# Kernel optimization log

Measured on AMD Instinct MI355X. Metric: run time of the kernel, lower is better.

Reference implementation:

```python
import jax, jax.numpy as jnp
import numpy as np
from jax import lax
from jax.scipy.special import gammaln

N, H, W = 16, 1080, 1920
NUM_SV = 600
KS, KSIG = 7, 7.0 / 6.0
GAMMA_NP = np.arange(0.2, 10.0 + 0.001, 0.001, dtype=np.float64).astype(np.float32)

FEATURE_RANGES = jnp.asarray([[0.338, 10], [0.017204, 0.806612], [0.236, 1.642], [-0.123884, 0.20293], [0.000155, 0.712298], [0.001122, 0.470257], [0.244, 1.641], [-0.123586, 0.179083], [0.000152, 0.710456], [0.000975, 0.470984], [0.249, 1.555], [-0.135687, 0.100858], [0.000174, 0.684173], [0.000913, 0.534174], [0.258, 1.561], [-0.143408, 0.100486], [0.000179, 0.685696], [0.000888, 0.536508], [0.471, 3.264], [0.012809, 0.703171], [0.218, 1.046], [-0.094876, 0.187459], [1.5e-05, 0.442057], [0.001272, 0.40803], [0.222, 1.042], [-0.115772, 0.162604], [1.6e-05, 0.444362], [0.001374, 0.40243], [0.227, 0.996], [-0.117188, 0.098323], [3e-05, 0.531903], [0.001122, 0.369589], [0.228, 0.99], [-0.12243, 0.098658], [2.8e-05, 0.530092], [0.001118, 0.370399]], dtype=jnp.float32)


def _gauss_kernel():
    ax = np.arange(KS, dtype=np.float64) - (KS - 1) / 2
    g = np.exp(-(ax ** 2) / (2 * KSIG ** 2))
    k = np.outer(g, g)
    k /= k.sum()
    return jnp.asarray(k, jnp.float32)


def _cubic(x):
    ax = np.abs(x); ax2 = ax * ax; ax3 = ax2 * ax
    return (1.5 * ax3 - 2.5 * ax2 + 1) * (ax <= 1) + (-0.5 * ax3 + 2.5 * ax2 - 4 * ax + 2) * ((ax > 1) & (ax <= 2))


def _resize_matrix(in_len, scale=0.5):
    # Matlab-style antialiased bicubic downscale weights as a dense (out,in) matrix.
    out_len = int(np.ceil(in_len * scale))
    kw = 4.0 / scale
    u = (np.arange(1, out_len + 1, dtype=np.float64) / scale) + 0.5 * (1 - 1 / scale)
    left = np.floor(u - kw / 2)
    P = int(np.ceil(kw)) + 2
    ind = left[:, None] + np.arange(P)[None, :]  # 1-based
    w = scale * _cubic((u[:, None] - ind) * scale)
    w = w / w.sum(1, keepdims=True)
    aux = np.concatenate([np.arange(in_len), np.arange(in_len)[::-1]])  # symmetric boundary
    idx = aux[np.mod(ind.astype(np.int64) - 1, 2 * in_len)]
    M = np.zeros((out_len, in_len), np.float64)
    np.add.at(M, (np.repeat(np.arange(out_len), P), idx.ravel()), w.ravel())
    return jnp.asarray(M, jnp.float32)


def imresize_half(x):
    Mh = _resize_matrix(x.shape[-2])
    Mw = _resize_matrix(x.shape[-1])
    x = jnp.einsum('oh,nchw->ncow', Mh, x)
    return jnp.einsum('pw,ncow->ncop', Mw, x)


def normalize_img_with_gauss(x):
    k = _gauss_kernel()[None, None]  # (1,1,7,7)
    conv = lambda z: lax.conv_general_dilated(z, k, (1, 1), 'SAME', dimension_numbers=('NCHW', 'OIHW', 'NCHW'))
    mu = conv(x)
    sigma = jnp.sqrt(jnp.abs(conv(x * x) - mu * mu) + 1e-8)
    return (x - mu) / (sigma + 1.0)


def _tables():
    g = jnp.asarray(GAMMA_NP)
    r = jnp.exp(2 * gammaln(2.0 / g) - gammaln(1.0 / g) - gammaln(3.0 / g))
    return g, r


def estimate_ggd(x):
    g, r = _tables()
    s2 = jnp.mean(x * x, axis=(1, 2, 3))
    E = jnp.mean(jnp.abs(x), axis=(1, 2, 3))
    rho = s2 / (E * E)
    idx = jnp.argmin(jnp.abs(rho[:, None] - r[None, :]), axis=-1)
    return g[idx], jnp.sqrt(s2)


def estimate_aggd(x):
    g, r = _tables()
    ml = (x < 0).astype(x.dtype)
    mr = (x > 0).astype(x.dtype)
    cl = jnp.sum(ml, (1, 2, 3))
    cr = jnp.sum(mr, (1, 2, 3))
    sl = jnp.sqrt(jnp.sum((x * ml) ** 2, (1, 2, 3)) / cl)
    sr = jnp.sqrt(jnp.sum((x * mr) ** 2, (1, 2, 3)) / cr)
    gh = sl / sr
    rhat = jnp.mean(jnp.abs(x), (1, 2, 3)) ** 2 / jnp.mean(x * x, (1, 2, 3))
    rhn = rhat * (gh ** 3 + 1) * (gh + 1) / (gh ** 2 + 1) ** 2
    idx = jnp.argmin(jnp.abs(r[None, :] - rhn[:, None]), axis=-1)
    return g[idx], sl, sr


def natural_scene_statistics(luma):
    xn = normalize_img_with_gauss(luma)
    a, s = estimate_ggd(xn)
    feats = [a, s * s]
    for sh in ((0, 1), (1, 0), (1, 1), (-1, 1)):
        xs = jnp.roll(xn, sh, axis=(-2, -1))
        a, sl, sr = estimate_aggd(xn * xs)
        eta = (sr - sl) * jnp.exp(gammaln(2.0 / a) - (gammaln(1.0 / a) + gammaln(3.0 / a)) / 2)
        feats += [a, eta, sl * sl, sr * sr]
    return jnp.stack(feats, -1)  # (N,18)


def setup_inputs() -> dict:
    key = jax.random.key(0)
    k1, k2, k3 = jax.random.split(key, 3)
    x = jax.random.uniform(k1, (N, 3, H, W), jnp.float32)
    sv = jax.random.normal(k2, (NUM_SV, 36), jnp.float32)
    sv_coef = jax.random.normal(k3, (NUM_SV,), jnp.float32)
    return {'x': x, 'sv': sv, 'sv_coef': sv_coef}


def reference(x, sv, sv_coef):
    # Y channel (YIQ luma, pyiqa default), scaled to [0,255]
    y = jnp.einsum('nchw,c->nhw', x, jnp.asarray([0.299, 0.587, 0.114], x.dtype))[:, None] * 255.0
    f1 = natural_scene_statistics(y)
    f2 = natural_scene_statistics(imresize_half(y))
    f = jnp.concatenate([f1, f2], axis=-1)  # (N,36)
    lo = FEATURE_RANGES[:, 0]
    hi = FEATURE_RANGES[:, 1]
    sf = -1.0 + 2.0 * (f - lo) / (hi - lo)
    dist = jnp.sum((sf[:, :, None] - sv.T[None, :, :]) ** 2, axis=1)  # (N,num_sv)
    kf = jnp.exp(-0.05 * dist)
    return kf @ sv_coef + 153.591  # score = kf@coef - rho, rho=-153.591
```

## Files before the change

### kernel.cpp

```cpp
#include <hip/hip_runtime.h>
#include <math.h>

#define NIMG 16
#define FH 1080
#define FW 1920
#define HHh 540
#define HWw 960
#define FHW (FH*FW)
#define TMPW (HHh*FW)
#define HHW (HHh*HWw)
#define NG 9801

struct GW { float w[7]; };

__device__ const float FR[36][2] = {
 {0.338f, 10.f}, {0.017204f, 0.806612f}, {0.236f, 1.642f}, {-0.123884f, 0.20293f},
 {0.000155f, 0.712298f}, {0.001122f, 0.470257f}, {0.244f, 1.641f}, {-0.123586f, 0.179083f},
 {0.000152f, 0.710456f}, {0.000975f, 0.470984f}, {0.249f, 1.555f}, {-0.135687f, 0.100858f},
 {0.000174f, 0.684173f}, {0.000913f, 0.534174f}, {0.258f, 1.561f}, {-0.143408f, 0.100486f},
 {0.000179f, 0.685696f}, {0.000888f, 0.536508f}, {0.471f, 3.264f}, {0.012809f, 0.703171f},
 {0.218f, 1.046f}, {-0.094876f, 0.187459f}, {1.5e-05f, 0.442057f}, {0.001272f, 0.40803f},
 {0.222f, 1.042f}, {-0.115772f, 0.162604f}, {1.6e-05f, 0.444362f}, {0.001374f, 0.40243f},
 {0.227f, 0.996f}, {-0.117188f, 0.098323f}, {3e-05f, 0.531903f}, {0.001122f, 0.369589f},
 {0.228f, 0.99f}, {-0.12243f, 0.098658f}, {2.8e-05f, 0.530092f}, {0.001118f, 0.370399f}
};

__global__ void k_zero(float* p, int n){
  int i = blockIdx.x*blockDim.x + threadIdx.x;
  if (i < n) p[i] = 0.f;
}

__global__ __launch_bounds__(256) void k_luma(const float* __restrict__ x, float* __restrict__ y, int n0, int nb){
  long long idx = (long long)blockIdx.x*blockDim.x + threadIdx.x;
  long long tot = (long long)nb*(FHW/4);
  if (idx >= tot) return;
  int n = (int)(idx / (FHW/4));
  int p = (int)(idx - (long long)n*(FHW/4));
  const float4* base = (const float4*)(x + (long long)(n0+n)*3*FHW);
  float4 r = base[p];
  float4 g = base[p + FHW/4];
  float4 b = base[p + 2*(FHW/4)];
  float4 o;
  o.x = 255.0f*(0.299f*r.x + 0.587f*g.x + 0.114f*b.x);
  o.y = 255.0f*(0.299f*r.y + 0.587f*g.y + 0.114f*b.y);
  o.z = 255.0f*(0.299f*r.z + 0.587f*g.z + 0.114f*b.z);
  o.w = 255.0f*(0.299f*r.w + 0.587f*g.w + 0.114f*b.w);
  ((float4*)(y + (long long)n*FHW))[p] = o;
}

__global__ __launch_bounds__(256) void k_gnorm(const float* __restrict__ src, float* __restrict__ dst,
                                               int Hi, int Wi, GW gw){
  __shared__ float ly[38][40];
  __shared__ float hs[38][33];
  __shared__ float h2[38][33];
  int n = blockIdx.z;
  const float* im = src + (long long)n*Hi*Wi;
  float* om = dst + (long long)n*Hi*Wi;
  int bx = blockIdx.x*32, by = blockIdx.y*32;
  int tid = threadIdx.x;
  for (int t = tid; t < 38*38; t += 256){
    int r = t / 38, c = t - r*38;
    int gi = by + r - 3, gj = bx + c - 3;
    float v = 0.f;
    if (gi >= 0 && gi < Hi && gj >= 0 && gj < Wi) v = im[(long long)gi*Wi + gj];
    ly[r][c] = v;
  }
  __syncthreads();
  for (int t = tid; t < 38*32; t += 256){
    int r = t >> 5, c = t & 31;
    float s = 0.f, s2 = 0.f;
    #pragma unroll
    for (int k = 0; k < 7; k++){ float v = ly[r][c+k]; s += gw.w[k]*v; s2 += gw.w[k]*v*v; }
    hs[r][c] = s; h2[r][c] = s2;
  }
  __syncthreads();
  int c = tid & 31, r0 = tid >> 5;
  for (int r = r0; r < 32; r += 8){
    float mu = 0.f, m2 = 0.f;
    #pragma unroll
    for (int k = 0; k < 7; k++){ mu += gw.w[k]*hs[r+k][c]; m2 += gw.w[k]*h2[r+k][c]; }
    int gi = by + r, gj = bx + c;
    if (gi < Hi && gj < Wi){
      float yv = ly[r+3][c+3];
      float sig = sqrtf(fabsf(m2 - mu*mu) + 1e-8f);
      om[(long long)gi*Wi + gj] = (yv - mu)/(sig + 1.0f);
    }
  }
}

__global__ __launch_bounds__(256) void k_nss(const float* __restrict__ xn, float* __restrict__ acc,
                                             int Hi, int Wi, int accBase){
  int n = blockIdx.y;
  const float* img = xn + (long long)n*Hi*Wi;
  float a[22];
  #pragma unroll
  for (int k = 0; k < 22; k++) a[k] = 0.f;
  for (int i = blockIdx.x; i < Hi; i += gridDim.x){
    const float* rc = img + (long long)i*Wi;
    const float* rm = img + (long long)((i==0)?(Hi-1):(i-1))*Wi;
    const float* rp = img + (long long)((i==Hi-1)?0:(i+1))*Wi;
    for (int j = threadIdx.x; j < Wi; j += 256){
      int jm = (j==0)?(Wi-1):(j-1);
      float xc = rc[j];
      float xl = rc[jm], xu = rm[j], xul = rm[jm], xdl = rp[jm];
      a[0] += xc*xc;
      a[1] += fabsf(xc);
      float pr[4] = {xc*xl, xc*xu, xc*xul, xc*xdl};
      #pragma unroll
      for (int k = 0; k < 4; k++){
        float pp = pr[k];
        float q = pp*pp;
        if (pp < 0.f){ a[2+5*k] += 1.f; a[4+5*k] += q; }
        else if (pp > 0.f){ a[3+5*k] += 1.f; a[5+5*k] += q; }
        a[6+5*k] += fabsf(pp);
      }
    }
  }
  __shared__ float wsum[4][22];
  int lane = threadIdx.x & 63, wv = threadIdx.x >> 6;
  #pragma unroll
  for (int k = 0; k < 22; k++){
    float v = a[k];
    for (int off = 32; off > 0; off >>= 1) v += __shfl_down(v, off, 64);
    if (lane == 0) wsum[wv][k] = v;
  }
  __syncthreads();
  if (threadIdx.x < 22){
    float s = wsum[0][threadIdx.x]+wsum[1][threadIdx.x]+wsum[2][threadIdx.x]+wsum[3][threadIdx.x];
    atomicAdd(&acc[accBase + n*22 + threadIdx.x], s);
  }
}

__device__ double d_cubic(double x){
  double ax = fabs(x), ax2 = ax*ax, ax3 = ax2*ax;
  if (ax <= 1.0) return 1.5*ax3 - 2.5*ax2 + 1.0;
  if (ax <= 2.0) return -0.5*ax3 + 2.5*ax2 - 4.0*ax + 2.0;
  return 0.0;
}

__global__ void k_rsetup(float* __restrict__ wH, int* __restrict__ iH,
                         float* __restrict__ wW, int* __restrict__ iW){
  int t = blockIdx.x*blockDim.x + threadIdx.x;
  int inl, o; float* wp; int* ip;
  if (t < HHh){ inl = FH; wp = wH; ip = iH; o = t; }
  else if (t < HHh + HWw){ inl = FW; wp = wW; ip = iW; o = t - HHh; }
  else return;
  double u = 2.0*(o+1) - 0.5;
  double left = floor(u - 4.0);
  double wv[10]; int idx[10]; double s = 0.0;
  for (int p = 0; p < 10; p++){
    double ind = left + p;
    double xv = (u - ind)*0.5;
    double w = 0.5*d_cubic(xv);
    wv[p] = w; s += w;
    long long L2 = 2*(long long)inl;
    long long m = (long long)ind - 1;
    m = ((m % L2) + L2) % L2;
    idx[p] = (m < inl) ? (int)m : (int)(L2 - 1 - m);
  }
  for (int p = 0; p < 10; p++){
    wp[o*10+p] = (float)(wv[p]/s);
    ip[o*10+p] = idx[p];
  }
}

__global__ __launch_bounds__(256) void k_resizeh(const float* __restrict__ y, float* __restrict__ tmp,
                                                 const float* __restrict__ wH, const int* __restrict__ iH, int nb){
  int t = blockIdx.x*blockDim.x + threadIdx.x;
  int tot = nb*HHh*(FW/4);
  if (t >= tot) return;
  int j = t % (FW/4);
  int o = (t / (FW/4)) % HHh;
  int n = t / (HHh*(FW/4));
  const float* yi = y + (long long)n*FHW;
  float4 s = {0.f,0.f,0.f,0.f};
  for (int p = 0; p < 10; p++){
    float w = wH[o*10+p];
    int r = iH[o*10+p];
    float4 v = ((const float4*)(yi + (long long)r*FW))[j];
    s.x += w*v.x; s.y += w*v.y; s.z += w*v.z; s.w += w*v.w;
  }
  ((float4*)(tmp + (long long)n*TMPW))[o*(FW/4)+j] = s;
}

__global__ __launch_bounds__(256) void k_resizew(const float* __restrict__ tmp, float* __restrict__ yh,
                                                 const float* __restrict__ wW, const int* __restrict__ iW, int nb){
  int t = blockIdx.x*blockDim.x + threadIdx.x;
  int tot = nb*HHW;
  if (t >= tot) return;
  int q = t % HWw;
  int o = (t / HWw) % HHh;
  int n = t / HHW;
  const float* row = tmp + (long long)n*TMPW + (long long)o*FW;
  float s = 0.f;
  for (int p = 0; p < 10; p++) s += wW[q*10+p]*row[iW[q*10+p]];
  yh[(long long)n*HHW + (long long)o*HWw + q] = s;
}

__global__ void k_rtab(float* __restrict__ rt){
  int i = blockIdx.x*blockDim.x + threadIdx.x;
  if (i >= NG) return;
  float g = (float)(0.2 + 0.001*(double)i);
  double gd = (double)g;
  double r = exp(2.0*lgamma(2.0/gd) - lgamma(1.0/gd) - lgamma(3.0/gd));
  rt[i] = (float)r;
}

__global__ __launch_bounds__(256) void k_final(const float* __restrict__ acc, const float* __restrict__ rt,
                                               const float* __restrict__ sv, const float* __restrict__ coef,
                                               float* __restrict__ out){
  int n = blockIdx.x;
  __shared__ float targ[10];
  __shared__ float sfs[36];
  __shared__ int argi[10];
  __shared__ float slv[8], srv[8], feat[36];
  __shared__ float rbv[4]; __shared__ int rbi[4];
  __shared__ float ws2[4];
  int tid = threadIdx.x;
  if (tid == 0){
    for (int s = 0; s < 2; s++){
      const float* A = acc + (s*NIMG + n)*22;
      double HWs = s ? (double)HHW : (double)FHW;
      double s2m = A[0]/HWs;
      double Em  = A[1]/HWs;
      targ[s*5+0] = (float)(s2m/(Em*Em));
      feat[s*18+1] = (float)s2m;
      for (int k = 0; k < 4; k++){
        double cl = A[2+5*k], cr = A[3+5*k], sl2 = A[4+5*k], sr2 = A[5+5*k], sab = A[6+5*k];
        double sl = sqrt(sl2/cl), sr = sqrt(sr2/cr);
        double gh = sl/sr;
        double rhat = (sab/HWs)*(sab/HWs)/((sl2+sr2)/HWs);
        double rhn = rhat*(gh*gh*gh + 1.0)*(gh + 1.0)/((gh*gh + 1.0)*(gh*gh + 1.0));
        targ[s*5+1+k] = (float)rhn;
        slv[s*4+k] = (float)sl; srv[s*4+k] = (float)sr;
        feat[s*18+2+4*k+2] = (float)(sl2/cl);
        feat[s*18+2+4*k+3] = (float)(sr2/cr);
      }
    }
  }
  __syncthreads();
  for (int tix = 0; tix < 10; tix++){
    float tv = targ[tix];
    float bv = 3.4e38f; int bi = 0;
    for (int i = tid; i < NG; i += 256){
      float d = fabsf(tv - rt[i]);
      if (d < bv){ bv = d; bi = i; }
    }
    for (int off = 32; off > 0; off >>= 1){
      float ov = __shfl_down(bv, off, 64);
      int   oi = __shfl_down(bi, off, 64);
      if (ov < bv || (ov == bv && oi < bi)){ bv = ov; bi = oi; }
    }
    int lane = tid & 63, wv = tid >> 6;
    if (lane == 0){ rbv[wv] = bv; rbi[wv] = bi; }
    __syncthreads();
    if (tid == 0){
      for (int w = 1; w < 4; w++)
        if (rbv[w] < bv || (rbv[w] == bv && rbi[w] < bi)){ bv = rbv[w]; bi = rbi[w]; }
      argi[tix] = bi;
    }
    __syncthreads();
  }
  if (tid == 0){
    for (int s = 0; s < 2; s++){
      feat[s*18+0] = (float)(0.2 + 0.001*(double)argi[s*5]);
      for (int k = 0; k < 4; k++){
        double a = 0.2 + 0.001*(double)argi[s*5+1+k];
        double e = exp(lgamma(2.0/a) - 0.5*(lgamma(1.0/a) + lgamma(3.0/a)));
        feat[s*18+2+4*k+0] = (float)a;
        feat[s*18+2+4*k+1] = (float)(((double)srv[s*4+k] - (double)slv[s*4+k])*e);
      }
    }
    for (int i = 0; i < 36; i++){
      float lo = FR[i][0], hi = FR[i][1];
      sfs[i] = -1.0f + 2.0f*(feat[i]-lo)/(hi-lo);
    }
  }
  __syncthreads();
  float local = 0.f;
  for (int v = tid; v < 600; v += 256){
    float d = 0.f;
    #pragma unroll 4
    for (int i = 0; i < 36; i++){ float df = sfs[i] - sv[v*36+i]; d += df*df; }
    local += expf(-0.05f*d)*coef[v];
  }
  for (int off = 32; off > 0; off >>= 1) local += __shfl_down(local, off, 64);
  int lane = tid & 63, wv = tid >> 6;
  if (lane == 0) ws2[wv] = local;
  __syncthreads();
  if (tid == 0) out[n] = ws2[0]+ws2[1]+ws2[2]+ws2[3] + 153.591f;
}

extern "C" void kernel_launch(void* const* d_in, const int* in_sizes, int n_in,
                              void* d_out, int out_size, void* d_ws, size_t ws_size,
                              hipStream_t stream){
  const float* x    = (const float*)d_in[0];
  const float* sv   = (const float*)d_in[1];
  const float* coef = (const float*)d_in[2];
  float* out = (float*)d_out;
  char* ws = (char*)d_ws;

  float* acc = (float*)(ws + 0);
  float* rt  = (float*)(ws + 4096);
  float* wH  = (float*)(ws + 49152);
  int*   iH  = (int*)  (ws + 73728);
  float* wW  = (float*)(ws + 98304);
  int*   iW  = (int*)  (ws + 139264);
  float* Ybuf = (float*)(ws + 262144);

  size_t big = (ws_size > 262144) ? ws_size - 262144 : 0;
  int nbmax = (int)(big / (2ull*FHW*4));
  if (nbmax < 1) nbmax = 1;
  if (nbmax > NIMG) nbmax = NIMG;
  float* Bbuf = Ybuf + (size_t)nbmax*FHW;

  GW gw;
  {
    double g[7], s = 0.0;
    for (int k = 0; k < 7; k++){ double d = k - 3; g[k] = exp(-d*d/(2.0*(7.0/6.0)*(7.0/6.0))); s += g[k]; }
    for (int k = 0; k < 7; k++) gw.w[k] = (float)(g[k]/s);
  }

  k_zero<<<4, 256, 0, stream>>>(acc, 704);
  k_rtab<<<(NG+255)/256, 256, 0, stream>>>(rt);
  k_rsetup<<<(HHh+HWw+255)/256, 256, 0, stream>>>(wH, iH, wW, iW);

  for (int n0 = 0; n0 < NIMG; n0 += nbmax){
    int nb = (NIMG - n0 < nbmax) ? (NIMG - n0) : nbmax;
    {
      long long tot = (long long)nb*(FHW/4);
      k_luma<<<(int)((tot+255)/256), 256, 0, stream>>>(x, Ybuf, n0, nb);
    }
    {
      dim3 g2((FW+31)/32, (FH+31)/32, nb);
      k_gnorm<<<g2, 256, 0, stream>>>(Ybuf, Bbuf, FH, FW, gw);
    }
    k_nss<<<dim3(64, nb), 256, 0, stream>>>(Bbuf, acc, FH, FW, (0*NIMG + n0)*22);
    {
      int tot = nb*HHh*(FW/4);
      k_resizeh<<<(tot+255)/256, 256, 0, stream>>>(Ybuf, Bbuf, wH, iH, nb);
    }
    {
      int tot = nb*HHW;
      k_resizew<<<(tot+255)/256, 256, 0, stream>>>(Bbuf, Ybuf, wW, iW, nb);
    }
    float* XNH = Bbuf + (size_t)nbmax*TMPW;
    {
      dim3 g2((HWw+31)/32, (HHh+31)/32, nb);
      k_gnorm<<<g2, 256, 0, stream>>>(Ybuf, XNH, HHh, HWw, gw);
    }
    k_nss<<<dim3(64, nb), 256, 0, stream>>>(XNH, acc, HHh, HWw, (1*NIMG + n0)*22);
  }

  k_final<<<NIMG, 256, 0, stream>>>(acc, rt, sv, coef, out);
}
```

Measured before the change: 1.059 ms.

## Fuse Gaussian normalization with NSS statistics and fix wraparound borders separately

Merges the local-mean/variance normalization kernel and the paired-product statistics kernel into one tiled kernel. Each tile now computes a 34x34 normalized patch in shared memory and accumulates the 22 moments directly, so the normalized image is never written to or read back from global memory. Circular-wraparound border pairs are handled by a separate strip and fixup pass that recomputes the normalized values of the edge rows and columns. Atomics are spread over 32 slots per image to reduce contention, and the final kernel sums the slots. It also adds float4 tile loads for interior tiles. The cost is extra halo recompute per tile and more kernel launches for the small border passes.

```diff
diff --git a/kernel.cpp b/kernel.cpp
--- a/kernel.cpp
+++ b/kernel.cpp
@@ -10,6 +10,7 @@
 #define TMPW (HHh*FW)
 #define HHW (HHh*HWw)
 #define NG 9801
+#define NSLOT 32
 
 struct GW { float w[7]; };
 
@@ -48,86 +49,203 @@
   ((float4*)(y + (long long)n*FHW))[p] = o;
 }
 
-__global__ __launch_bounds__(256) void k_gnorm(const float* __restrict__ src, float* __restrict__ dst,
-                                               int Hi, int Wi, GW gw){
-  __shared__ float ly[38][40];
-  __shared__ float hs[38][33];
-  __shared__ float h2[38][33];
+__global__ __launch_bounds__(256) void k_fused(const float* __restrict__ src, float* __restrict__ acc,
+                                               int Hi, int Wi, int accBase, GW gw){
+  __shared__ float ly[40][48];
+  __shared__ float hs[40][36];
+  __shared__ float h2[40][36];
+  __shared__ float xs[34][36];
+  __shared__ float wsum[4][22];
   int n = blockIdx.z;
   const float* im = src + (long long)n*Hi*Wi;
-  float* om = dst + (long long)n*Hi*Wi;
   int bx = blockIdx.x*32, by = blockIdx.y*32;
   int tid = threadIdx.x;
-  for (int t = tid; t < 38*38; t += 256){
-    int r = t / 38, c = t - r*38;
-    int gi = by + r - 3, gj = bx + c - 3;
-    float v = 0.f;
-    if (gi >= 0 && gi < Hi && gj >= 0 && gj < Wi) v = im[(long long)gi*Wi + gj];
-    ly[r][c] = v;
-  }
-  __syncthreads();
-  for (int t = tid; t < 38*32; t += 256){
-    int r = t >> 5, c = t & 31;
-    float s = 0.f, s2 = 0.f;
-    #pragma unroll
-    for (int k = 0; k < 7; k++){ float v = ly[r][c+k]; s += gw.w[k]*v; s2 += gw.w[k]*v*v; }
-    hs[r][c] = s; h2[r][c] = s2;
-  }
-  __syncthreads();
-  int c = tid & 31, r0 = tid >> 5;
-  for (int r = r0; r < 32; r += 8){
-    float mu = 0.f, m2 = 0.f;
-    #pragma unroll
-    for (int k = 0; k < 7; k++){ mu += gw.w[k]*hs[r+k][c]; m2 += gw.w[k]*h2[r+k][c]; }
-    int gi = by + r, gj = bx + c;
-    if (gi < Hi && gj < Wi){
-      float yv = ly[r+3][c+3];
-      float sig = sqrtf(fabsf(m2 - mu*mu) + 1e-8f);
-      om[(long long)gi*Wi + gj] = (yv - mu)/(sig + 1.0f);
-    }
-  }
-}
-
-__global__ __launch_bounds__(256) void k_nss(const float* __restrict__ xn, float* __restrict__ acc,
-                                             int Hi, int Wi, int accBase){
+  bool fast = (bx >= 4) && (bx+36 <= Wi) && (by >= 4) && (by+36 <= Hi);
+  if (fast){
+    const float* base = im + (long long)(by-4)*Wi + (bx-4);
+    for (int t = tid; t < 400; t += 256){
+      int r = t/10, q = t-10*r;
+      float4 v = *(const float4*)(base + (long long)r*Wi + 4*q);
+      *(float4*)&ly[r][4*q] = v;
+    }
+  } else {
+    for (int t = tid; t < 1600; t += 256){
+      int r = t/40, c = t-40*r;
+      int gi = by-4+r, gj = bx-4+c;
+      float v = 0.f;
+      if (gi>=0 && gi<Hi && gj>=0 && gj<Wi) v = im[(long long)gi*Wi+gj];
+      ly[r][c] = v;
+    }
+  }
+  __syncthreads();
+  for (int t = tid; t < 360; t += 256){
+    int r = t/9, g = t-9*r; int c0 = 4*g;
+    float v[10];
+    #pragma unroll
+    for (int k=0;k<10;k++) v[k] = ly[r][c0+k];
+    #pragma unroll
+    for (int q=0;q<4;q++){
+      int cg = c0+q;
+      if (cg < 34){
+        float s=0.f, s2=0.f;
+        #pragma unroll
+        for (int k=0;k<7;k++){ float yv=v[q+k]; s += gw.w[k]*yv; s2 += gw.w[k]*yv*yv; }
+        hs[r][cg]=s; h2[r][cg]=s2;
+      }
+    }
+  }
+  __syncthreads();
+  for (int t = tid; t < 306; t += 256){
+    int rg0 = t/34, c = t-34*rg0; int r0 = 4*rg0;
+    float a[10], b[10];
+    #pragma unroll
+    for (int k=0;k<10;k++){
+      int rr = r0+k;
+      if (rr < 40){ a[k]=hs[rr][c]; b[k]=h2[rr][c]; } else { a[k]=0.f; b[k]=0.f; }
+    }
+    #pragma unroll
+    for (int q=0;q<4;q++){
+      int rg = r0+q;
+      if (rg < 34){
+        float mu=0.f, m2=0.f;
+        #pragma unroll
+        for (int k=0;k<7;k++){ mu += gw.w[k]*a[q+k]; m2 += gw.w[k]*b[q+k]; }
+        float yv = ly[rg+3][c+3];
+        float sig = sqrtf(fabsf(m2-mu*mu)+1e-8f);
+        xs[rg][c] = (yv-mu)/(sig+1.f);
+      }
+    }
+  }
+  __syncthreads();
+  float aR[22];
+  #pragma unroll
+  for (int k=0;k<22;k++) aR[k]=0.f;
+  {
+    int pc = tid & 31, rg = tid >> 5;
+    int r0 = 4*rg;
+    float xL[6], xC[6];
+    #pragma unroll
+    for (int k=0;k<6;k++){ xL[k]=xs[r0+k][pc]; xC[k]=xs[r0+k][pc+1]; }
+    int j = bx+pc;
+    #pragma unroll
+    for (int q=0;q<4;q++){
+      int i = by + r0 + q;
+      if (i < Hi && j < Wi){
+        float xc = xC[q+1];
+        aR[0] += xc*xc; aR[1] += fabsf(xc);
+        if (i != 0 && i != Hi-1 && j != 0){
+          float pr4[4] = { xc*xL[q+1], xc*xC[q], xc*xL[q], xc*xL[q+2] };
+          #pragma unroll
+          for (int k=0;k<4;k++){
+            float pp = pr4[k]; float qq = pp*pp;
+            if (pp<0.f){ aR[2+5*k]+=1.f; aR[4+5*k]+=qq; }
+            else if (pp>0.f){ aR[3+5*k]+=1.f; aR[5+5*k]+=qq; }
+            aR[6+5*k]+=fabsf(pp);
+          }
+        }
+      }
+    }
+  }
+  int lane = tid & 63, wv = tid >> 6;
+  #pragma unroll
+  for (int k=0;k<22;k++){
+    float v = aR[k];
+    for (int off=32; off>0; off>>=1) v += __shfl_down(v, off, 64);
+    if (lane==0) wsum[wv][k]=v;
+  }
+  __syncthreads();
+  if (tid < 22){
+    float s = wsum[0][tid]+wsum[1][tid]+wsum[2][tid]+wsum[3][tid];
+    int slot = (blockIdx.x + blockIdx.y) & (NSLOT-1);
+    atomicAdd(&acc[(((long long)(accBase + n))*NSLOT + slot)*22 + tid], s);
+  }
+}
+
+__device__ float xn_at(const float* __restrict__ im, int Hi, int Wi, int i, int j, const GW& gw){
+  float mu=0.f, m2=0.f;
+  for (int kr=-3;kr<=3;kr++){
+    int ii=i+kr; if (ii<0||ii>=Hi) continue;
+    float wr = gw.w[kr+3];
+    const float* row = im + (long long)ii*Wi;
+    for (int kc=-3;kc<=3;kc++){
+      int jj=j+kc; if (jj<0||jj>=Wi) continue;
+      float w = wr*gw.w[kc+3];
+      float yv = row[jj];
+      mu += w*yv; m2 += w*yv*yv;
+    }
+  }
+  float yv = im[(long long)i*Wi+j];
+  float sig = sqrtf(fabsf(m2-mu*mu)+1e-8f);
+  return (yv-mu)/(sig+1.f);
+}
+
+__global__ __launch_bounds__(256) void k_strips(const float* __restrict__ src, float* __restrict__ strip,
+                                                int Hi, int Wi, GW gw){
   int n = blockIdx.y;
-  const float* img = xn + (long long)n*Hi*Wi;
-  float a[22];
+  const float* im = src + (long long)n*Hi*Wi;
+  int C = 4*Wi + 2*Hi;
+  float* sb = strip + (long long)n*C;
+  for (int u = blockIdx.x*256 + threadIdx.x; u < C; u += gridDim.x*256){
+    int i, j;
+    if (u < 4*Wi){ int r=u/Wi; j=u-r*Wi; i = (r==0)?0:(r==1)?1:(r==2)?(Hi-2):(Hi-1); }
+    else { int v=u-4*Wi; int c=v/Hi; i=v-c*Hi; j = c?(Wi-1):0; }
+    sb[u] = xn_at(im, Hi, Wi, i, j, gw);
+  }
+}
+
+__device__ float strip_get(const float* __restrict__ sb, int Hi, int Wi, int i, int j){
+  if (i==0)    return sb[j];
+  if (i==1)    return sb[Wi+j];
+  if (i==Hi-2) return sb[2*Wi+j];
+  if (i==Hi-1) return sb[3*Wi+j];
+  if (j==0)    return sb[4*Wi+i];
+  return sb[4*Wi+Hi+i];
+}
+
+__global__ __launch_bounds__(256) void k_fixup(const float* __restrict__ strip, float* __restrict__ acc,
+                                               int Hi, int Wi, int accBase){
+  int n = blockIdx.y;
+  int C = 4*Wi + 2*Hi;
+  const float* sb = strip + (long long)n*C;
+  int nB = 2*Wi + Hi - 2;
+  float aR[20];
   #pragma unroll
-  for (int k = 0; k < 22; k++) a[k] = 0.f;
-  for (int i = blockIdx.x; i < Hi; i += gridDim.x){
-    const float* rc = img + (long long)i*Wi;
-    const float* rm = img + (long long)((i==0)?(Hi-1):(i-1))*Wi;
-    const float* rp = img + (long long)((i==Hi-1)?0:(i+1))*Wi;
-    for (int j = threadIdx.x; j < Wi; j += 256){
-      int jm = (j==0)?(Wi-1):(j-1);
-      float xc = rc[j];
-      float xl = rc[jm], xu = rm[j], xul = rm[jm], xdl = rp[jm];
-      a[0] += xc*xc;
-      a[1] += fabsf(xc);
-      float pr[4] = {xc*xl, xc*xu, xc*xul, xc*xdl};
-      #pragma unroll
-      for (int k = 0; k < 4; k++){
-        float pp = pr[k];
-        float q = pp*pp;
-        if (pp < 0.f){ a[2+5*k] += 1.f; a[4+5*k] += q; }
-        else if (pp > 0.f){ a[3+5*k] += 1.f; a[5+5*k] += q; }
-        a[6+5*k] += fabsf(pp);
-      }
-    }
-  }
-  __shared__ float wsum[4][22];
+  for (int k=0;k<20;k++) aR[k]=0.f;
+  for (int u = blockIdx.x*256 + threadIdx.x; u < nB; u += gridDim.x*256){
+    int i, j;
+    if (u < Wi){ i=0; j=u; }
+    else if (u < 2*Wi){ i=Hi-1; j=u-Wi; }
+    else { i = u-2*Wi+1; j=0; }
+    int jm = (j==0)?(Wi-1):(j-1);
+    int im_ = (i==0)?(Hi-1):(i-1);
+    int ip = (i==Hi-1)?0:(i+1);
+    float xc  = strip_get(sb,Hi,Wi,i,j);
+    float xl  = strip_get(sb,Hi,Wi,i,jm);
+    float xu  = strip_get(sb,Hi,Wi,im_,j);
+    float xul = strip_get(sb,Hi,Wi,im_,jm);
+    float xdl = strip_get(sb,Hi,Wi,ip,jm);
+    float pr4[4] = { xc*xl, xc*xu, xc*xul, xc*xdl };
+    #pragma unroll
+    for (int k=0;k<4;k++){
+      float pp = pr4[k]; float qq = pp*pp;
+      if (pp<0.f){ aR[0+5*k]+=1.f; aR[2+5*k]+=qq; }
+      else if (pp>0.f){ aR[1+5*k]+=1.f; aR[3+5*k]+=qq; }
+      aR[4+5*k]+=fabsf(pp);
+    }
+  }
+  __shared__ float wsum[4][20];
   int lane = threadIdx.x & 63, wv = threadIdx.x >> 6;
   #pragma unroll
-  for (int k = 0; k < 22; k++){
-    float v = a[k];
-    for (int off = 32; off > 0; off >>= 1) v += __shfl_down(v, off, 64);
-    if (lane == 0) wsum[wv][k] = v;
-  }
-  __syncthreads();
-  if (threadIdx.x < 22){
+  for (int k=0;k<20;k++){
+    float v = aR[k];
+    for (int off=32; off>0; off>>=1) v += __shfl_down(v, off, 64);
+    if (lane==0) wsum[wv][k]=v;
+  }
+  __syncthreads();
+  if (threadIdx.x < 20){
     float s = wsum[0][threadIdx.x]+wsum[1][threadIdx.x]+wsum[2][threadIdx.x]+wsum[3][threadIdx.x];
-    atomicAdd(&acc[accBase + n*22 + threadIdx.x], s);
+    int slot = blockIdx.x & (NSLOT-1);
+    atomicAdd(&acc[(((long long)(accBase + n))*NSLOT + slot)*22 + 2 + threadIdx.x], s);
   }
 }
 
@@ -210,6 +328,7 @@
                                                const float* __restrict__ sv, const float* __restrict__ coef,
                                                float* __restrict__ out){
   int n = blockIdx.x;
+  __shared__ float A[44];
   __shared__ float targ[10];
   __shared__ float sfs[36];
   __shared__ int argi[10];
@@ -217,16 +336,24 @@
   __shared__ float rbv[4]; __shared__ int rbi[4];
   __shared__ float ws2[4];
   int tid = threadIdx.x;
+  if (tid < 44){
+    int s = tid/22, k = tid-22*s;
+    const float* p = acc + (((long long)(s*NIMG + n))*NSLOT)*22 + k;
+    float sum = 0.f;
+    for (int sl = 0; sl < NSLOT; sl++) sum += p[sl*22];
+    A[tid] = sum;
+  }
+  __syncthreads();
   if (tid == 0){
     for (int s = 0; s < 2; s++){
-      const float* A = acc + (s*NIMG + n)*22;
+      const float* Ap = A + s*22;
       double HWs = s ? (double)HHW : (double)FHW;
-      double s2m = A[0]/HWs;
-      double Em  = A[1]/HWs;
+      double s2m = Ap[0]/HWs;
+      double Em  = Ap[1]/HWs;
       targ[s*5+0] = (float)(s2m/(Em*Em));
       feat[s*18+1] = (float)s2m;
       for (int k = 0; k < 4; k++){
-        double cl = A[2+5*k], cr = A[3+5*k], sl2 = A[4+5*k], sr2 = A[5+5*k], sab = A[6+5*k];
+        double cl = Ap[2+5*k], cr = Ap[3+5*k], sl2 = Ap[4+5*k], sr2 = Ap[5+5*k], sab = Ap[6+5*k];
         double sl = sqrt(sl2/cl), sr = sqrt(sr2/cr);
         double gh = sl/sr;
         double rhat = (sab/HWs)*(sab/HWs)/((sl2+sr2)/HWs);
@@ -300,19 +427,24 @@
   float* out = (float*)d_out;
   char* ws = (char*)d_ws;
 
-  float* acc = (float*)(ws + 0);
-  float* rt  = (float*)(ws + 4096);
-  float* wH  = (float*)(ws + 49152);
-  int*   iH  = (int*)  (ws + 73728);
-  float* wW  = (float*)(ws + 98304);
-  int*   iW  = (int*)  (ws + 139264);
-  float* Ybuf = (float*)(ws + 262144);
-
-  size_t big = (ws_size > 262144) ? ws_size - 262144 : 0;
-  int nbmax = (int)(big / (2ull*FHW*4));
+  float* acc    = (float*)(ws + 0);
+  float* rt     = (float*)(ws + 98304);
+  float* wH     = (float*)(ws + 139264);
+  int*   iH     = (int*)  (ws + 163840);
+  float* wW     = (float*)(ws + 188416);
+  int*   iW     = (int*)  (ws + 229376);
+  float* stripF = (float*)(ws + 270336);
+  float* stripH = (float*)(ws + 901120);
+  float* big    = (float*)(ws + 1310720);
+
+  size_t bigbytes = (ws_size > 1310720) ? ws_size - 1310720 : 0;
+  size_t perimg = (size_t)(FHW + TMPW + HHW)*4;
+  int nbmax = (int)(bigbytes / perimg);
   if (nbmax < 1) nbmax = 1;
   if (nbmax > NIMG) nbmax = NIMG;
-  float* Bbuf = Ybuf + (size_t)nbmax*FHW;
+  float* Ybuf = big;
+  float* Tbuf = Ybuf + (size_t)nbmax*FHW;
+  float* Hbuf = Tbuf + (size_t)nbmax*TMPW;
 
   GW gw;
   {
@@ -321,7 +453,7 @@
     for (int k = 0; k < 7; k++) gw.w[k] = (float)(g[k]/s);
   }
 
-  k_zero<<<4, 256, 0, stream>>>(acc, 704);
+  k_zero<<<(22528+255)/256, 256, 0, stream>>>(acc, 22528);
   k_rtab<<<(NG+255)/256, 256, 0, stream>>>(rt);
   k_rsetup<<<(HHh+HWw+255)/256, 256, 0, stream>>>(wH, iH, wW, iW);
 
@@ -333,23 +465,32 @@
     }
     {
       dim3 g2((FW+31)/32, (FH+31)/32, nb);
-      k_gnorm<<<g2, 256, 0, stream>>>(Ybuf, Bbuf, FH, FW, gw);
-    }
-    k_nss<<<dim3(64, nb), 256, 0, stream>>>(Bbuf, acc, FH, FW, (0*NIMG + n0)*22);
+      k_fused<<<g2, 256, 0, stream>>>(Ybuf, acc, FH, FW, 0*NIMG + n0, gw);
+    }
+    {
+      int C = 4*FW + 2*FH;
+      k_strips<<<dim3((C+255)/256, nb), 256, 0, stream>>>(Ybuf, stripF, FH, FW, gw);
+      int nB = 2*FW + FH - 2;
+      k_fixup<<<dim3((nB+255)/256, nb), 256, 0, stream>>>(stripF, acc, FH, FW, 0*NIMG + n0);
+    }
     {
       int tot = nb*HHh*(FW/4);
-      k_resizeh<<<(tot+255)/256, 256, 0, stream>>>(Ybuf, Bbuf, wH, iH, nb);
+      k_resizeh<<<(tot+255)/256, 256, 0, stream>>>(Ybuf, Tbuf, wH, iH, nb);
     }
     {
       int tot = nb*HHW;
-      k_resizew<<<(tot+255)/256, 256, 0, stream>>>(Bbuf, Ybuf, wW, iW, nb);
-    }
-    float* XNH = Bbuf + (size_t)nbmax*TMPW;
+      k_resizew<<<(tot+255)/256, 256, 0, stream>>>(Tbuf, Hbuf, wW, iW, nb);
+    }
     {
       dim3 g2((HWw+31)/32, (HHh+31)/32, nb);
-      k_gnorm<<<g2, 256, 0, stream>>>(Ybuf, XNH, HHh, HWw, gw);
-    }
-    k_nss<<<dim3(64, nb), 256, 0, stream>>>(XNH, acc, HHh, HWw, (1*NIMG + n0)*22);
+      k_fused<<<g2, 256, 0, stream>>>(Hbuf, acc, HHh, HWw, 1*NIMG + n0, gw);
+    }
+    {
+      int C = 4*HWw + 2*HHh;
+      k_strips<<<dim3((C+255)/256, nb), 256, 0, stream>>>(Hbuf, stripH, HHh, HWw, gw);
+      int nB = 2*HWw + HHh - 2;
+      k_fixup<<<dim3((nB+255)/256, nb), 256, 0, stream>>>(stripH, acc, HHh, HWw, 1*NIMG + n0);
+    }
   }
 
   k_final<<<NIMG, 256, 0, stream>>>(acc, rt, sv, coef, out);
```

New measurement: 1.192 ms. +12.6%, slower.
